# Optimization experiments

Measured on AMD Instinct MI355X. Metric: run time of the kernel, lower is better.

The kernel has to match this reference:

```python
import jax, jax.numpy as jnp
import numpy as np

B, C, N, H = 4, 256, 1024, 8
D = C            # per-head q/k dim (out_channels defaults to in_channels)
DV = C           # per-head value/output dim (y_out_channels defaults to out_channels)


def setup_inputs() -> dict:
    key = jax.random.key(0)
    ks = jax.random.split(key, 10)
    s = 0.02
    return {
        "x": jax.random.normal(ks[0], (B, C, N), jnp.float32),
        "y": jax.random.normal(ks[1], (B, C, N), jnp.float32),
        "Wq": jax.random.normal(ks[2], (H * D, C), jnp.float32) * s,
        "bq": jnp.zeros((H * D,), jnp.float32),
        "Wk": jax.random.normal(ks[3], (H * D, C), jnp.float32) * s,
        "bk": jnp.zeros((H * D,), jnp.float32),
        "Wv": jax.random.normal(ks[4], (H * DV, C), jnp.float32) * s,
        "bv": jnp.zeros((H * DV,), jnp.float32),
        "Wp": jax.random.normal(ks[5], (DV, C), jnp.float32) * s,  # projection, bias=False
        "gamma": jax.random.uniform(ks[6], (H, 1, 1, 1), jnp.float32) + 0.001,
    }


def _pconv(t, W, b):
    # 1x1 conv1d: (O,C) x (B,C,N) -> (B,O,N)
    out = jnp.einsum('oc,bcn->bon', W, t)
    return out if b is None else out + b[None, :, None]


def reference(x, y, Wq, bq, Wk, bk, Wv, bv, Wp, gamma):
    b_, _, n_ = x.shape
    h = gamma.shape[0]
    # Q/K/V projections, split channels into h heads (head-major chunks of D)
    q = _pconv(x, Wq, bq).reshape(b_, h, -1, n_)   # [B,H,D,N]
    k = _pconv(x, Wk, bk).reshape(b_, h, -1, n_)   # [B,H,D,N]
    v = _pconv(y, Wv, bv).reshape(b_, h, -1, n_)   # [B,H,DV,N]
    # energy[i,j] = sum_d q[d,i]*k[d,j]; softmax over keys j (no sqrt(d) scaling)
    attn = jax.nn.softmax(jnp.einsum('bhdn,bhdm->bhnm', q, k), axis=-1)
    out = jnp.einsum('bhdm,bhnm->bhdn', v, attn)   # [B,H,DV,N]
    # residual branch: y projected to DV channels (1x1 conv, no bias)
    yp = jnp.einsum('oc,bcn->bon', Wp, y)          # [B,DV,N]
    g = gamma.reshape(1, h, 1, 1)
    out = (g * out + yp[:, None, :, :]) / (1.0 + g)
    # concat heads along channel dim (head-major), matching split_cat(out,1,0,2)
    return out.reshape(b_, -1, n_)                 # [B,H*DV,N]
```

## Files before the change

kernel.cpp:

```cpp
#include <hip/hip_runtime.h>

#define Bb 4
#define Cc 256
#define Nn 1024
#define Hh 8
#define Oo 2048

typedef __attribute__((ext_vector_type(8))) short bf16x8;
typedef __attribute__((ext_vector_type(4))) float f32x4;

__device__ __forceinline__ short f2bf(float f) {
  unsigned u = __builtin_bit_cast(unsigned, f);
  unsigned r = u + 0x7FFFu + ((u >> 16) & 1u);
  return (short)(r >> 16);
}
__device__ __forceinline__ f32x4 mfma16(bf16x8 a, bf16x8 b, f32x4 c) {
  return __builtin_amdgcn_mfma_f32_16x16x32_bf16(a, b, c, 0, 0, 0);
}
__device__ __forceinline__ void gl_lds16(const void* g, void* l) {
  __builtin_amdgcn_global_load_lds(
      (const __attribute__((address_space(1))) void*)g,
      (__attribute__((address_space(3))) void*)l, 16, 0, 0);
}

__device__ __forceinline__ void stage_row512(const char* gbase, char* lds,
                                             int wave, int lane) {
#pragma unroll
  for (int i = 0; i < 8; i++) {
    int off = (wave * 8 + i) * 1024;
    int L = off + lane * 16;
    int r = L >> 9;
    int c = ((L >> 4) & 31) ^ (r & 7);
    gl_lds16(gbase + r * 512 + c * 16, lds + off);
  }
}
__device__ __forceinline__ void stage_v(const char* Vg, char* lds, int k0,
                                        int wave, int lane) {
#pragma unroll
  for (int i = 0; i < 8; i++) {
    int off = (wave * 8 + i) * 1024;
    int L = off + lane * 16;
    int r = L >> 7;
    int c = ((L >> 4) & 7) ^ (r & 7);
    gl_lds16(Vg + (size_t)r * 2048 + k0 * 2 + c * 16, lds + off);
  }
}

__global__ __launch_bounds__(256) void k_transpose(
    const float* __restrict__ x, const float* __restrict__ y,
    short* __restrict__ xT, short* __restrict__ yT,
    const float* __restrict__ Wq, const float* __restrict__ Wk,
    const float* __restrict__ Wv, const float* __restrict__ Wp,
    short* __restrict__ dWq, short* __restrict__ dWk, short* __restrict__ dWv,
    short* __restrict__ dWp) {
  {
    const int NW = Oo * Cc;
    int lin = blockIdx.x + 16 * (blockIdx.y + 4 * blockIdx.z);
    for (int i = (lin * 256 + threadIdx.x) * 4; i < 3 * NW + Cc * Cc;
         i += 512 * 256 * 4) {
      const float* src;
      short* dst;
      int off;
      if (i < NW) {
        src = Wq; dst = dWq; off = i;
      } else if (i < 2 * NW) {
        src = Wk; dst = dWk; off = i - NW;
      } else if (i < 3 * NW) {
        src = Wv; dst = dWv; off = i - 2 * NW;
      } else {
        src = Wp; dst = dWp; off = i - 3 * NW;
      }
      float4 v = *(const float4*)(src + off);
      short4 o;
      o.x = f2bf(v.x);
      o.y = f2bf(v.y);
      o.z = f2bf(v.z);
      o.w = f2bf(v.w);
      *(short4*)(dst + off) = o;
    }
  }
  int bz = blockIdx.z;
  int b = bz >> 1;
  const float* src = (bz & 1) ? y : x;
  short* dst = (bz & 1) ? yT : xT;
  src += (size_t)b * Cc * Nn;
  dst += (size_t)b * Nn * Cc;
  __shared__ short tile[64][72];
  int n0 = blockIdx.x * 64, c0 = blockIdx.y * 64;
  int t = threadIdx.x;
#pragma unroll
  for (int i = 0; i < 16; i++) {
    int idx = t + i * 256;
    int cc = idx >> 6, nn = idx & 63;
    tile[cc][nn] = f2bf(src[(size_t)(c0 + cc) * Nn + n0 + nn]);
  }
  __syncthreads();
#pragma unroll
  for (int i = 0; i < 16; i++) {
    int idx = t + i * 256;
    int nn = idx >> 6, cc = idx & 63;
    dst[(size_t)(n0 + nn) * Cc + c0 + cc] = tile[cc][nn];
  }
}

__global__ __launch_bounds__(256) void k_proj_qk(
    const short* __restrict__ xT, const short* __restrict__ Wq,
    const float* __restrict__ bq, const short* __restrict__ Wk,
    const float* __restrict__ bk, short* __restrict__ Qt,
    short* __restrict__ Kt) {
  int b = blockIdx.z, n0 = blockIdx.x * 64, o0 = blockIdx.y * 64;
  int wave = threadIdx.x >> 6, lane = threadIdx.x & 63;
  int quad = lane >> 4, l16 = lane & 15;
  int sw = l16 & 7;
  __shared__ short Wqs[64 * 256];
  __shared__ short Wks[64 * 256];

  stage_row512((const char*)(Wq + (size_t)o0 * Cc), (char*)Wqs, wave, lane);
  stage_row512((const char*)(Wk + (size_t)o0 * Cc), (char*)Wks, wave, lane);
  const short* aptr =
      xT + (size_t)b * Nn * Cc + (size_t)(n0 + wave * 16 + l16) * Cc + quad * 8;
  bf16x8 areg[8];
#pragma unroll
  for (int ks = 0; ks < 8; ks++) areg[ks] = *(const bf16x8*)(aptr + ks * 32);

  f32x4 accQ[4], accK[4];
#pragma unroll
  for (int j = 0; j < 4; j++) {
    accQ[j] = f32x4{0.f, 0.f, 0.f, 0.f};
    accK[j] = f32x4{0.f, 0.f, 0.f, 0.f};
  }
  __syncthreads();
#pragma unroll
  for (int ks = 0; ks < 8; ks++) {
#pragma unroll
    for (int cj = 0; cj < 4; cj++) {
      int off = (cj * 16 + l16) * 512 + (((ks * 4 + quad) ^ sw) << 4);
      bf16x8 wqf = *(const bf16x8*)((const char*)Wqs + off);
      bf16x8 wkf = *(const bf16x8*)((const char*)Wks + off);
      accQ[cj] = mfma16(wqf, areg[ks], accQ[cj]);
      accK[cj] = mfma16(wkf, areg[ks], accK[cj]);
    }
  }
#pragma unroll
  for (int cj = 0; cj < 4; cj++) {
    int obase = o0 + cj * 16 + quad * 4;
    int h = obase >> 8, d = obase & 255;
    int n = n0 + wave * 16 + l16;
    float4 vbq = *(const float4*)(bq + obase);
    float4 vbk = *(const float4*)(bk + obase);
    size_t idx = (((size_t)(b * Hh + h) * Nn) + n) * 256 + d;
    short4 oq, ok;
    oq.x = f2bf(accQ[cj][0] + vbq.x);
    oq.y = f2bf(accQ[cj][1] + vbq.y);
    oq.z = f2bf(accQ[cj][2] + vbq.z);
    oq.w = f2bf(accQ[cj][3] + vbq.w);
    ok.x = f2bf(accK[cj][0] + vbk.x);
    ok.y = f2bf(accK[cj][1] + vbk.y);
    ok.z = f2bf(accK[cj][2] + vbk.z);
    ok.w = f2bf(accK[cj][3] + vbk.w);
    *(short4*)(Qt + idx) = oq;
    *(short4*)(Kt + idx) = ok;
  }
}

__global__ __launch_bounds__(256) void k_proj_v(
    const short* __restrict__ yTs, const short* __restrict__ Wv,
    const float* __restrict__ bv, const short* __restrict__ Wp,
    short* __restrict__ Vv, float* __restrict__ yp) {
  int b = blockIdx.z, n0 = blockIdx.x * 64;
  int by = blockIdx.y;
  bool isP = by >= 32;
  const short* W = isP ? Wp : Wv;
  int o0 = (isP ? (by - 32) : by) * 64;
  int wave = threadIdx.x >> 6, lane = threadIdx.x & 63;
  int quad = lane >> 4, l16 = lane & 15;
  int sw = l16 & 7;
  __shared__ short Ys[64 * 256];

  stage_row512((const char*)(yTs + (size_t)b * Nn * Cc + (size_t)n0 * Cc),
               (char*)Ys, wave, lane);
  const short* aptr = W + (size_t)(o0 + wave * 16 + l16) * Cc + quad * 8;
  bf16x8 areg[8];
#pragma unroll
  for (int ks = 0; ks < 8; ks++) areg[ks] = *(const bf16x8*)(aptr + ks * 32);

  f32x4 acc[4];
#pragma unroll
  for (int j = 0; j < 4; j++) acc[j] = f32x4{0.f, 0.f, 0.f, 0.f};
  __syncthreads();
#pragma unroll
  for (int ks = 0; ks < 8; ks++) {
#pragma unroll
    for (int cj = 0; cj < 4; cj++) {
      bf16x8 bb = *(const bf16x8*)((const char*)Ys + (cj * 16 + l16) * 512 +
                                   (((ks * 4 + quad) ^ sw) << 4));
      acc[cj] = mfma16(areg[ks], bb, acc[cj]);
    }
  }
#pragma unroll
  for (int cj = 0; cj < 4; cj++) {
    int n = n0 + cj * 16 + l16;
#pragma unroll
    for (int r = 0; r < 4; r++) {
      int o = o0 + wave * 16 + quad * 4 + r;
      if (isP) {
        yp[((size_t)b * Cc + o) * Nn + n] = acc[cj][r];
      } else {
        float v = acc[cj][r] + bv[o];
        Vv[((size_t)b * Oo + o) * Nn + n] = f2bf(v);
      }
    }
  }
}

__global__ __launch_bounds__(256) void k_attn(
    const short* __restrict__ Qt, const short* __restrict__ Kt,
    const short* __restrict__ Vv, const float* __restrict__ yp,
    const float* __restrict__ gamma, float* __restrict__ out) {
  int id = blockIdx.x;
  int bh = (id & 7) * 4 + (id >> 7);
  int q0 = ((id >> 3) & 15) * 64;
  int b = bh >> 3, h = bh & 7;
  int wave = threadIdx.x >> 6, lane = threadIdx.x & 63;
  int quad = lane >> 4, l16 = lane & 15;
  int sw = l16 & 7;
  const short* Qb = Qt + (size_t)bh * Nn * 256;
  const char* Kg = (const char*)(Kt + (size_t)bh * Nn * 256);
  const char* Vg = (const char*)(Vv + (size_t)bh * 256 * Nn);

  __shared__ short Klds[64 * 256];
  __shared__ short Vlds[256 * 64];
  __shared__ short plds[4][16][64];
  __shared__ float llds[64];

  bf16x8 qreg[8];
  {
    const short* qp = Qb + (size_t)(q0 + wave * 16 + l16) * 256 + quad * 8;
#pragma unroll
    for (int ks = 0; ks < 8; ks++) qreg[ks] = *(const bf16x8*)(qp + ks * 32);
  }
  f32x4 oacc[16];
#pragma unroll
  for (int j = 0; j < 16; j++) oacc[j] = f32x4{0.f, 0.f, 0.f, 0.f};
  float l_i[4] = {0.f, 0.f, 0.f, 0.f};

  stage_row512(Kg, (char*)Klds, wave, lane);
  stage_v(Vg, (char*)Vlds, 0, wave, lane);

  for (int kt = 0; kt < 16; kt++) {
    int k0 = kt * 64;
    asm volatile("s_waitcnt vmcnt(8)" ::: "memory");
    __builtin_amdgcn_s_barrier();
    __builtin_amdgcn_sched_barrier(0);
    f32x4 sc[4];
#pragma unroll
    for (int j = 0; j < 4; j++) sc[j] = f32x4{0.f, 0.f, 0.f, 0.f};
    __builtin_amdgcn_s_setprio(1);
#pragma unroll
    for (int ks = 0; ks < 8; ks++) {
#pragma unroll
      for (int cj = 0; cj < 4; cj++) {
        bf16x8 kb = *(const bf16x8*)((const char*)Klds +
                                     (cj * 16 + l16) * 512 +
                                     (((ks * 4 + quad) ^ sw) << 4));
        sc[cj] = mfma16(qreg[ks], kb, sc[cj]);
      }
    }
    __builtin_amdgcn_s_setprio(0);
#pragma unroll
    for (int cj = 0; cj < 4; cj++) {
#pragma unroll
      for (int r = 0; r < 4; r++) {
        float p = __expf(sc[cj][r]);
        l_i[r] += p;
        int row = quad * 4 + r;
        plds[wave][row][(((cj * 2 + (l16 >> 3)) ^ (row & 7)) << 3) | sw] =
            f2bf(p);
      }
    }
    asm volatile("s_waitcnt vmcnt(0) lgkmcnt(0)" ::: "memory");
    __builtin_amdgcn_s_barrier();
    __builtin_amdgcn_sched_barrier(0);
    if (kt < 15)
      stage_row512(Kg + (size_t)(k0 + 64) * 512, (char*)Klds, wave, lane);
    bf16x8 ap0[4], ap1[4];
#pragma unroll
    for (int qb = 0; qb < 4; qb++) {
      ap0[qb] = *(const bf16x8*)&plds[qb][l16][(quad ^ sw) << 3];
      ap1[qb] = *(const bf16x8*)&plds[qb][l16][((quad + 4) ^ sw) << 3];
    }
    __builtin_amdgcn_s_setprio(1);
#pragma unroll
    for (int dj = 0; dj < 4; dj++) {
      const char* vrow = (const char*)Vlds + (wave * 64 + dj * 16 + l16) * 128;
      bf16x8 v0 = *(const bf16x8*)(vrow + ((quad ^ sw) << 4));
      bf16x8 v1 = *(const bf16x8*)(vrow + (((quad + 4) ^ sw) << 4));
#pragma unroll
      for (int qb = 0; qb < 4; qb++) {
        oacc[qb * 4 + dj] = mfma16(ap0[qb], v0, oacc[qb * 4 + dj]);
        oacc[qb * 4 + dj] = mfma16(ap1[qb], v1, oacc[qb * 4 + dj]);
      }
    }
    __builtin_amdgcn_s_setprio(0);
    asm volatile("s_waitcnt lgkmcnt(0)" ::: "memory");
    __builtin_amdgcn_s_barrier();
    __builtin_amdgcn_sched_barrier(0);
    if (kt < 15) stage_v(Vg, (char*)Vlds, k0 + 64, wave, lane);
  }
#pragma unroll
  for (int r = 0; r < 4; r++) {
    float v = l_i[r];
    v += __shfl_xor(v, 1);
    v += __shfl_xor(v, 2);
    v += __shfl_xor(v, 4);
    v += __shfl_xor(v, 8);
    l_i[r] = v;
  }
  if (l16 == 0) {
    f32x4 lv;
#pragma unroll
    for (int r = 0; r < 4; r++) lv[r] = l_i[r];
    *(f32x4*)&llds[wave * 16 + quad * 4] = lv;
  }
  __syncthreads();
  float gf = gamma[h];
  float sg = gf / (1.f + gf), sy = 1.f / (1.f + gf);
#pragma unroll
  for (int qb = 0; qb < 4; qb++) {
    f32x4 lv = *(const f32x4*)&llds[qb * 16 + quad * 4];
    int qq = q0 + qb * 16 + quad * 4;
#pragma unroll
    for (int dj = 0; dj < 4; dj++) {
      int dv = wave * 64 + dj * 16 + l16;
      const float* ypp = yp + ((size_t)b * 256 + dv) * Nn + qq;
      float* op = out + ((size_t)b * Oo + h * 256 + dv) * Nn + qq;
      float4 yv = *(const float4*)ypp;
      f32x4 oa = oacc[qb * 4 + dj];
      float4 ov;
      ov.x = sg * (oa[0] / lv[0]) + sy * yv.x;
      ov.y = sg * (oa[1] / lv[1]) + sy * yv.y;
      ov.z = sg * (oa[2] / lv[2]) + sy * yv.z;
      ov.w = sg * (oa[3] / lv[3]) + sy * yv.w;
      *(float4*)op = ov;
    }
  }
}

extern "C" void kernel_launch(void* const* d_in, const int* in_sizes, int n_in,
                              void* d_out, int out_size, void* d_ws,
                              size_t ws_size, hipStream_t stream) {
  const float* x = (const float*)d_in[0];
  const float* y = (const float*)d_in[1];
  const float* Wq = (const float*)d_in[2];
  const float* bq = (const float*)d_in[3];
  const float* Wk = (const float*)d_in[4];
  const float* bk = (const float*)d_in[5];
  const float* Wv = (const float*)d_in[6];
  const float* bv = (const float*)d_in[7];
  const float* Wp = (const float*)d_in[8];
  const float* gamma = (const float*)d_in[9];
  float* out = (float*)d_out;

  char* w = (char*)d_ws;
  short* Qt = (short*)(w + 0);
  short* Kt = (short*)(w + 16777216);
  short* Vv = (short*)(w + 33554432);
  short* xT = (short*)(w + 50331648);
  short* yT = (short*)(w + 52428800);
  float* yp = (float*)(w + 54525952);
  short* Wqb = (short*)(w + 58720256);
  short* Wkb = (short*)(w + 59768832);
  short* Wvb = (short*)(w + 60817408);
  short* Wpb = (short*)(w + 61865984);

  k_transpose<<<dim3(Nn / 64, Cc / 64, 2 * Bb), dim3(256), 0, stream>>>(
      x, y, xT, yT, Wq, Wk, Wv, Wp, Wqb, Wkb, Wvb, Wpb);
  k_proj_qk<<<dim3(Nn / 64, Oo / 64, Bb), dim3(256), 0, stream>>>(
      xT, Wqb, bq, Wkb, bk, Qt, Kt);
  k_proj_v<<<dim3(Nn / 64, 36, Bb), dim3(256), 0, stream>>>(yT, Wvb, bv, Wpb,
                                                            Vv, yp);
  k_attn<<<dim3(512), dim3(256), 0, stream>>>(Qt, Kt, Vv, yp, gamma, out);
}
```

Baseline: 211.6 us.

## Load V tiles directly into registers instead of staging through LDS

V is no longer staged into shared memory with async global-to-LDS copies. Each wave now loads its own V fragments straight from global memory into registers at the start of each key tile, before the QK MFMAs. The explicit vmcnt waits, setprio hints and sched barriers are replaced by plain __syncthreads, and one barrier per iteration is removed. This frees LDS and removes a sync point, but exposes global load latency inside the loop. The per-lane 16-byte loads are also less coalesced.

```diff
diff --git a/kernel.cpp b/kernel.cpp
--- a/kernel.cpp
+++ b/kernel.cpp
@@ -32,17 +32,6 @@
     int r = L >> 9;
     int c = ((L >> 4) & 31) ^ (r & 7);
     gl_lds16(gbase + r * 512 + c * 16, lds + off);
-  }
-}
-__device__ __forceinline__ void stage_v(const char* Vg, char* lds, int k0,
-                                        int wave, int lane) {
-#pragma unroll
-  for (int i = 0; i < 8; i++) {
-    int off = (wave * 8 + i) * 1024;
-    int L = off + lane * 16;
-    int r = L >> 7;
-    int c = ((L >> 4) & 7) ^ (r & 7);
-    gl_lds16(Vg + (size_t)r * 2048 + k0 * 2 + c * 16, lds + off);
   }
 }
 
@@ -229,7 +218,6 @@
   const char* Vg = (const char*)(Vv + (size_t)bh * 256 * Nn);
 
   __shared__ short Klds[64 * 256];
-  __shared__ short Vlds[256 * 64];
   __shared__ short plds[4][16][64];
   __shared__ float llds[64];
 
@@ -239,23 +227,27 @@
 #pragma unroll
     for (int ks = 0; ks < 8; ks++) qreg[ks] = *(const bf16x8*)(qp + ks * 32);
   }
+  const char* vb = Vg + (size_t)(wave * 64 + l16) * 2048 + quad * 16;
   f32x4 oacc[16];
 #pragma unroll
   for (int j = 0; j < 16; j++) oacc[j] = f32x4{0.f, 0.f, 0.f, 0.f};
   float l_i[4] = {0.f, 0.f, 0.f, 0.f};
 
   stage_row512(Kg, (char*)Klds, wave, lane);
-  stage_v(Vg, (char*)Vlds, 0, wave, lane);
 
   for (int kt = 0; kt < 16; kt++) {
     int k0 = kt * 64;
-    asm volatile("s_waitcnt vmcnt(8)" ::: "memory");
-    __builtin_amdgcn_s_barrier();
-    __builtin_amdgcn_sched_barrier(0);
+    __syncthreads();
+    bf16x8 vf[8];
+#pragma unroll
+    for (int dj = 0; dj < 4; dj++) {
+      const char* vp = vb + (size_t)dj * 16 * 2048 + k0 * 2;
+      vf[dj * 2] = *(const bf16x8*)vp;
+      vf[dj * 2 + 1] = *(const bf16x8*)(vp + 64);
+    }
     f32x4 sc[4];
 #pragma unroll
     for (int j = 0; j < 4; j++) sc[j] = f32x4{0.f, 0.f, 0.f, 0.f};
-    __builtin_amdgcn_s_setprio(1);
 #pragma unroll
     for (int ks = 0; ks < 8; ks++) {
 #pragma unroll
@@ -266,7 +258,6 @@
         sc[cj] = mfma16(qreg[ks], kb, sc[cj]);
       }
     }
-    __builtin_amdgcn_s_setprio(0);
 #pragma unroll
     for (int cj = 0; cj < 4; cj++) {
 #pragma unroll
@@ -278,9 +269,7 @@
             f2bf(p);
       }
     }
-    asm volatile("s_waitcnt vmcnt(0) lgkmcnt(0)" ::: "memory");
-    __builtin_amdgcn_s_barrier();
-    __builtin_amdgcn_sched_barrier(0);
+    __syncthreads();
     if (kt < 15)
       stage_row512(Kg + (size_t)(k0 + 64) * 512, (char*)Klds, wave, lane);
     bf16x8 ap0[4], ap1[4];
@@ -289,23 +278,16 @@
       ap0[qb] = *(const bf16x8*)&plds[qb][l16][(quad ^ sw) << 3];
       ap1[qb] = *(const bf16x8*)&plds[qb][l16][((quad + 4) ^ sw) << 3];
     }
-    __builtin_amdgcn_s_setprio(1);
 #pragma unroll
     for (int dj = 0; dj < 4; dj++) {
-      const char* vrow = (const char*)Vlds + (wave * 64 + dj * 16 + l16) * 128;
-      bf16x8 v0 = *(const bf16x8*)(vrow + ((quad ^ sw) << 4));
-      bf16x8 v1 = *(const bf16x8*)(vrow + (((quad + 4) ^ sw) << 4));
+      bf16x8 v0 = vf[dj * 2];
+      bf16x8 v1 = vf[dj * 2 + 1];
 #pragma unroll
       for (int qb = 0; qb < 4; qb++) {
         oacc[qb * 4 + dj] = mfma16(ap0[qb], v0, oacc[qb * 4 + dj]);
         oacc[qb * 4 + dj] = mfma16(ap1[qb], v1, oacc[qb * 4 + dj]);
       }
     }
-    __builtin_amdgcn_s_setprio(0);
-    asm volatile("s_waitcnt lgkmcnt(0)" ::: "memory");
-    __builtin_amdgcn_s_barrier();
-    __builtin_amdgcn_sched_barrier(0);
-    if (kt < 15) stage_v(Vg, (char*)Vlds, k0 + 64, wave, lane);
   }
 #pragma unroll
   for (int r = 0; r < 4; r++) {
```

After: 208.4 us. No clear change (-1.5%).
